# Optimization experiments

Hardware: AMD Instinct MI355X
Metric: run time of the kernel (lower is better)

## Reference

```python
import jax, jax.numpy as jnp
import numpy as np

T_CONST = 0.1

def _hardtanh(w):
    # F.hardtanh(w, min_val=1e-10, max_val=1)
    return jnp.clip(w, 1e-10, 1.0)

def _forward(inp, hn, w_str2str, w_str2snr, w_m12m1, w_m12str, w_thal2m1,
             w_m12thal, w_thal2str, w_str2stn, w_stn2snr, w_snr2thal,
             str2str_fixed, inp_weight, mean_w, mean_b, std_w, std_b, hid_dim):
    H = hid_dim
    H5 = 5 * H
    Z = jnp.zeros((H, H), dtype=inp.dtype)
    n_inhib = int(0.3 * H)

    # Diagonal 'D' matrices realized as column scalings (D is diagonal)
    m12m1_d = jnp.concatenate([jnp.ones((H - n_inhib,)), -jnp.ones((n_inhib,))])

    # Block masks
    str2str_mask = jnp.zeros((H, H))
    m12str_mask = jnp.concatenate([jnp.ones((H, H - n_inhib)), jnp.zeros((H, n_inhib))], axis=1)
    str2stn_mask = jnp.concatenate([jnp.zeros((H, H // 2)), jnp.ones((H, H // 2))], axis=1)
    str2snr_mask = jnp.concatenate([jnp.ones((H, H // 2)), jnp.zeros((H, H // 2))], axis=1)

    # Region masks over the full 5H state
    thal_mask = jnp.concatenate([jnp.zeros((3 * H,)), jnp.ones((H,)), jnp.zeros((H,))])
    m1_mask = jnp.zeros((H5,))  # cat(zeros(4H), zeros(H)) in the source

    # Effective recurrent blocks (str2str_D = stn2snr_D = snr2thal_D = str2snr_D = -I)
    str2str_rec = -(str2str_mask * _hardtanh(w_str2str) + str2str_fixed)
    m12m1_rec = _hardtanh(w_m12m1) * m12m1_d[None, :]
    m12str_rec = m12str_mask * _hardtanh(w_m12str)
    str2snr_rec = -(str2snr_mask * _hardtanh(w_str2snr))
    thal2m1_rec = _hardtanh(w_thal2m1)
    m12thal_rec = _hardtanh(w_m12thal)
    thal2str_rec = _hardtanh(w_thal2str)
    str2stn_rec = str2stn_mask * _hardtanh(w_str2stn)
    stn2snr_rec = -_hardtanh(w_str2stn)  # NOTE: source uses str2stn weight here (faithful to original)
    snr2thal_rec = -_hardtanh(w_snr2thal)

    W_rec = jnp.concatenate([
        jnp.concatenate([str2str_rec, Z, Z, thal2str_rec, m12str_rec], axis=1),
        jnp.concatenate([str2stn_rec, Z, Z, Z, Z], axis=1),
        jnp.concatenate([str2snr_rec, stn2snr_rec, Z, Z, Z], axis=1),
        jnp.concatenate([Z, Z, snr2thal_rec, Z, m12thal_rec], axis=1),
        jnp.concatenate([Z, Z, Z, thal2m1_rec, m12m1_rec], axis=1),
    ], axis=0)  # [5H, 5H]

    # Precompute masked input drive for all timesteps: [T, B, 5H]
    u = jnp.einsum('bti,ih->tbh', inp, _hardtanh(inp_weight)) * thal_mask

    W_rec_T = W_rec.T

    def step(h, u_t):
        # (W_rec @ h.T).T == h @ W_rec.T
        h_new = jax.nn.relu((1.0 - T_CONST) * h + T_CONST * (h @ W_rec_T + u_t))
        return h_new, h_new

    _, hs = jax.lax.scan(step, hn[0], u)  # hs: [T, B, 5H]
    rnn_out = jnp.transpose(hs, (1, 0, 2))  # [B, T, 5H]
    hn_last = rnn_out[:, -1, :][None]  # [1, B, 5H]

    masked = rnn_out * m1_mask
    mean_out = masked @ mean_w + mean_b
    std_out = jnp.clip(masked @ std_w + std_b, -5.0, 10.0)
    return mean_out, std_out, rnn_out, hn_last


def setup_inputs() -> dict:
    H, B, T, I, A = 256, 64, 512, 4, 1
    H5 = 5 * H
    key = jax.random.key(0)
    ks = jax.random.split(key, 20)
    u01 = lambda k, shape, s: jax.random.uniform(k, shape, dtype=jnp.float32) * s
    inputs = {
        'inp': jax.random.uniform(ks[0], (B, T, I), dtype=jnp.float32),
        'hn': jnp.zeros((1, B, H5), dtype=jnp.float32),
        'w_str2str': u01(ks[1], (H, H), 0.01),
        'w_str2snr': u01(ks[2], (H, H), 0.01),
        'w_m12m1': u01(ks[3], (H, H), 0.01),
        'w_m12str': u01(ks[4], (H, H), 0.01),
        'w_thal2m1': u01(ks[5], (H, H), 0.01),
        'w_m12thal': u01(ks[6], (H, H), 0.01),
        'w_thal2str': u01(ks[7], (H, H), 0.01),
        'w_str2stn': u01(ks[8], (H, H), 0.01),
        'w_stn2snr': u01(ks[9], (H, H), 0.01),
        'w_snr2thal': u01(ks[10], (H, H), 0.01),
        'inp_weight': u01(ks[12], (I, H5), 0.1),
        'mean_w': jax.random.normal(ks[13], (H5, A), dtype=jnp.float32) * 0.02,
        'mean_b': jnp.zeros((A,), dtype=jnp.float32),
        'std_w': jax.random.normal(ks[14], (H5, A), dtype=jnp.float32) * 0.02,
        'std_b': jnp.zeros((A,), dtype=jnp.float32),
        'hid_dim': H,
    }
    keep = jax.random.bernoulli(ks[11], 0.15, (H, H)).astype(jnp.float32)
    inputs['str2str_fixed'] = u01(ks[15], (H, H), 0.01) * keep
    return inputs


def reference(inp, hn, w_str2str, w_str2snr, w_m12m1, w_m12str, w_thal2m1,
              w_m12thal, w_thal2str, w_str2stn, w_stn2snr, w_snr2thal,
              str2str_fixed, inp_weight, mean_w, mean_b, std_w, std_b, hid_dim):
    return _forward(inp, hn, w_str2str, w_str2snr, w_m12m1, w_m12str, w_thal2m1,
                    w_m12thal, w_thal2str, w_str2stn, w_stn2snr, w_snr2thal,
                    str2str_fixed, inp_weight, mean_w, mean_b, std_w, std_b, hid_dim)
```

## Files before the change

### kernel.cpp

```cpp
#include <hip/hip_runtime.h>

typedef unsigned short u16;
typedef unsigned long long u64;
typedef __bf16 v8bf __attribute__((ext_vector_type(8)));
typedef float f32x4 __attribute__((ext_vector_type(4)));
typedef u16 u16x4 __attribute__((ext_vector_type(4)));

#define H5 1280
#define TT 512
#define NBLK 80
#define SPL 81920

#define OFF_W0 0
#define OFF_W1 3276800
#define OFF_W2 6553600
#define OFF_HS 9830400
#define OFF_WIN 10813440
#define OFF_CNT 10817536

#define MFMA(a, b, c) __builtin_amdgcn_mfma_f32_16x16x32_bf16(a, b, c, 0, 0, 0)

__device__ __forceinline__ float htanh_(float x) {
  return fminf(fmaxf(x, 1e-10f), 1.0f);
}
__device__ __forceinline__ u16 f2b(float f) {
  unsigned u = __float_as_uint(f);
  return (u16)((u + 0x7fffu + ((u >> 16) & 1u)) >> 16);
}
__device__ __forceinline__ float b2f(u16 b) {
  return __uint_as_float(((unsigned)b) << 16);
}

__device__ __forceinline__ v8bf ald16(const u16* p) {
  union { u64 q[2]; v8bf v; } u;
  u.q[0] = __hip_atomic_load((const u64*)p, __ATOMIC_RELAXED, __HIP_MEMORY_SCOPE_AGENT);
  u.q[1] = __hip_atomic_load((const u64*)(p + 4), __ATOMIC_RELAXED, __HIP_MEMORY_SCOPE_AGENT);
  return u.v;
}
__device__ __forceinline__ void sth(u16* p, u16x4 v) {
  union { u16x4 s; u64 q; } u;
  u.s = v;
  __hip_atomic_store((u64*)p, u.q, __ATOMIC_RELAXED, __HIP_MEMORY_SCOPE_AGENT);
}

__global__ void build_w(const float* __restrict__ w_str2snr, const float* __restrict__ w_m12m1,
                        const float* __restrict__ w_m12str, const float* __restrict__ w_thal2m1,
                        const float* __restrict__ w_m12thal, const float* __restrict__ w_thal2str,
                        const float* __restrict__ w_str2stn, const float* __restrict__ w_snr2thal,
                        const float* __restrict__ fixedw, u16* __restrict__ W0,
                        u16* __restrict__ W1, u16* __restrict__ W2) {
  int idx = blockIdx.x * 256 + threadIdx.x;
  if (idx >= H5 * H5) return;
  int j = idx / H5, k = idx - j * H5;
  int jr = j >> 8, kr = k >> 8, kk = k & 255;
  int o = (j & 255) * 256 + kk;
  float w = 0.0f;
  if (jr == 0) {
    if (kr == 0) w = -fixedw[o];
    else if (kr == 3) w = htanh_(w_thal2str[o]);
    else if (kr == 4) w = (kk < 180) ? htanh_(w_m12str[o]) : 0.0f;
  } else if (jr == 1) {
    if (kr == 0) w = (kk >= 128) ? htanh_(w_str2stn[o]) : 0.0f;
  } else if (jr == 2) {
    if (kr == 0) w = (kk < 128) ? -htanh_(w_str2snr[o]) : 0.0f;
    else if (kr == 1) w = -htanh_(w_str2stn[o]);
  } else if (jr == 3) {
    if (kr == 2) w = -htanh_(w_snr2thal[o]);
    else if (kr == 4) w = htanh_(w_m12thal[o]);
  } else {
    if (kr == 3) w = htanh_(w_thal2m1[o]);
    else if (kr == 4) w = (kk < 180) ? htanh_(w_m12m1[o]) : -htanh_(w_m12m1[o]);
  }
  u16 c0 = f2b(w);  float r1 = w - b2f(c0);
  u16 c1 = f2b(r1); float r2 = r1 - b2f(c1);
  u16 c2 = f2b(r2);
  W0[idx] = c0; W1[idx] = c1; W2[idx] = c2;
}

__global__ void build_misc(const float* __restrict__ hn, const float* __restrict__ inp_weight,
                           const float* __restrict__ mean_b, const float* __restrict__ std_b,
                           float* __restrict__ out, u16* __restrict__ hs, float* __restrict__ Win) {
  int gid = blockIdx.x * 256 + threadIdx.x;
  if (gid < 65536) {
    out[gid] = (gid < 32768) ? mean_b[0] : fminf(10.0f, fmaxf(-5.0f, std_b[0]));
  } else if (gid < 65536 + SPL) {
    int i = gid - 65536;
    float v = hn[i];
    u16 c0 = f2b(v);  float r1 = v - b2f(c0);
    u16 c1 = f2b(r1); float r2 = r1 - b2f(c1);
    u16 c2 = f2b(r2);
    hs[i] = c0; hs[SPL + i] = c1; hs[2 * SPL + i] = c2;
  } else if (gid < 65536 + SPL + 1024) {
    int i = gid - 65536 - SPL;
    Win[i] = htanh_(inp_weight[(i >> 8) * H5 + 768 + (i & 255)]);
  }
}

template <int R> struct RC;
template <> struct RC<0> { static constexpr int kb[3] = {0, 768, 1024}; static constexpr int nch[3] = {8, 8, 8}; };
template <> struct RC<1> { static constexpr int kb[3] = {128, 0, 0};    static constexpr int nch[3] = {4, 0, 0}; };
template <> struct RC<2> { static constexpr int kb[3] = {0, 256, 0};    static constexpr int nch[3] = {4, 8, 0}; };
template <> struct RC<3> { static constexpr int kb[3] = {512, 1024, 0}; static constexpr int nch[3] = {8, 8, 0}; };
template <> struct RC<4> { static constexpr int kb[3] = {768, 1024, 0}; static constexpr int nch[3] = {8, 8, 0}; };

template <int R>
__device__ __forceinline__ f32x4 do_mm(const u16* __restrict__ hs_r, int b, int lk,
                                       const u16* __restrict__ w0r, const u16* __restrict__ w1r,
                                       const u16* __restrict__ w2r) {
  f32x4 A00 = {0.f, 0.f, 0.f, 0.f}, A01 = {0.f, 0.f, 0.f, 0.f}, A02 = {0.f, 0.f, 0.f, 0.f};
  f32x4 A10 = {0.f, 0.f, 0.f, 0.f}, A11 = {0.f, 0.f, 0.f, 0.f}, A20 = {0.f, 0.f, 0.f, 0.f};
#pragma unroll
  for (int q = 0; q < 3; ++q) {
    if (RC<R>::nch[q] > 0) {
      const int kbq = RC<R>::kb[q];
      const u16* hb = hs_r + (long)b * H5 + kbq + lk;
#pragma unroll
      for (int c = 0; c < RC<R>::nch[q]; ++c) {
        v8bf h0 = ald16(hb + c * 32);
        v8bf h1 = ald16(hb + SPL + c * 32);
        v8bf h2 = ald16(hb + 2 * SPL + c * 32);
        v8bf a0 = *(const v8bf*)(w0r + kbq + c * 32);
        v8bf a1 = *(const v8bf*)(w1r + kbq + c * 32);
        v8bf a2 = *(const v8bf*)(w2r + kbq + c * 32);
        A00 = MFMA(a0, h0, A00);
        A01 = MFMA(a0, h1, A01);
        A02 = MFMA(a0, h2, A02);
        A10 = MFMA(a1, h0, A10);
        A11 = MFMA(a1, h1, A11);
        A20 = MFMA(a2, h0, A20);
      }
    }
  }
  f32x4 acc;
#pragma unroll
  for (int rr = 0; rr < 4; ++rr)
    acc[rr] = ((A00[rr] + A10[rr]) + (A01[rr] + A11[rr])) + (A02[rr] + A20[rr]);
  return acc;
}

template <int R>
__device__ void pers_loop(int j0, int b, int lr, int hi, int lk,
                          const float* __restrict__ inp_b, const float* __restrict__ hn,
                          const u16* __restrict__ W0, const u16* __restrict__ W1,
                          const u16* __restrict__ W2, u16* __restrict__ hs,
                          float* __restrict__ rnn_b, float* __restrict__ hn_last,
                          const float* __restrict__ Win, unsigned* __restrict__ counter) {
  const long jrow = (long)(j0 + lr) * H5 + lk;
  const u16* w0r = W0 + jrow;
  const u16* w1r = W1 + jrow;
  const u16* w2r = W2 + jrow;

  float winreg[4][4];
  if constexpr (R == 3) {
#pragma unroll
    for (int i = 0; i < 4; ++i)
#pragma unroll
      for (int rr = 0; rr < 4; ++rr)
        winreg[i][rr] = Win[i * 256 + (j0 - 768) + hi * 4 + rr];
  }

  f32x4 hprev;
  {
    const float* hp = hn + (long)b * H5 + j0 + hi * 4;
#pragma unroll
    for (int rr = 0; rr < 4; ++rr) hprev[rr] = hp[rr];
  }

  const u64 ca = (u64)counter;

  for (int t = 0; t < TT; ++t) {
    const u16* hs_r = hs + (t & 1) * (3 * SPL);
    u16* hs_w = hs + ((t & 1) ^ 1) * (3 * SPL);

    f32x4 acc = do_mm<R>(hs_r, b, lk, w0r, w1r, w2r);

    if constexpr (R == 3) {
      const float* ip = inp_b + t * 4;
      float i0 = ip[0], i1 = ip[1], i2 = ip[2], i3 = ip[3];
#pragma unroll
      for (int rr = 0; rr < 4; ++rr)
        acc[rr] += i0 * winreg[0][rr] + i1 * winreg[1][rr] + i2 * winreg[2][rr] + i3 * winreg[3][rr];
    }

    f32x4 hnew;
#pragma unroll
    for (int rr = 0; rr < 4; ++rr)
      hnew[rr] = fmaxf(0.0f, 0.9f * hprev[rr] + 0.1f * acc[rr]);
    hprev = hnew;

    *(f32x4*)(rnn_b + (long)t * H5 + j0 + hi * 4) = hnew;

    if (t < TT - 1) {
      u16x4 s0, s1, s2;
#pragma unroll
      for (int rr = 0; rr < 4; ++rr) {
        float v = hnew[rr];
        u16 c0 = f2b(v);  float r1 = v - b2f(c0);
        u16 c1 = f2b(r1); float r2 = r1 - b2f(c1);
        s0[rr] = c0; s1[rr] = c1; s2[rr] = f2b(r2);
      }
      u16* hw = hs_w + (long)b * H5 + j0 + hi * 4;
      sth(hw, s0);
      sth(hw + SPL, s1);
      sth(hw + 2 * SPL, s2);

      asm volatile("s_waitcnt vmcnt(0)" ::: "memory");
      __syncthreads();
      if (threadIdx.x == 0) {
        unsigned old;
        asm volatile("global_atomic_add %0, %1, %2, off sc0 sc1\n\t"
                     "s_waitcnt vmcnt(0)"
                     : "=v"(old) : "v"(ca), "v"(1u) : "memory");
        const unsigned target = (unsigned)(t + 1) * NBLK;
        for (;;) {
          unsigned cur;
          asm volatile("global_load_dword %0, %1, off sc0 sc1\n\t"
                       "s_waitcnt vmcnt(0)"
                       : "=v"(cur) : "v"(ca) : "memory");
          if (cur >= target) break;
          __builtin_amdgcn_s_sleep(1);
        }
      }
      __syncthreads();
    } else {
      float* hl = hn_last + (long)b * H5 + j0 + hi * 4;
#pragma unroll
      for (int rr = 0; rr < 4; ++rr) hl[rr] = hnew[rr];
    }
  }
}

__global__ void __launch_bounds__(256, 1)
rnn_pers(const float* __restrict__ inp, const float* __restrict__ hn,
         const u16* __restrict__ W0, const u16* __restrict__ W1, const u16* __restrict__ W2,
         u16* __restrict__ hs, float* __restrict__ rnn, float* __restrict__ hn_last,
         const float* __restrict__ Win, unsigned* __restrict__ counter) {
  const int lane = threadIdx.x & 63;
  const int lr = lane & 15, hi = lane >> 4, lk = hi * 8;
  const int jt = blockIdx.x;
  const int bt = threadIdx.x >> 6;
  const int j0 = jt << 4;
  const int b = (bt << 4) + lr;
  float* rnn_b = rnn + (long)b * TT * H5;
  const float* inp_b = inp + (long)b * TT * 4;
  switch (jt >> 4) {
    case 0: pers_loop<0>(j0, b, lr, hi, lk, inp_b, hn, W0, W1, W2, hs, rnn_b, hn_last, Win, counter); break;
    case 1: pers_loop<1>(j0, b, lr, hi, lk, inp_b, hn, W0, W1, W2, hs, rnn_b, hn_last, Win, counter); break;
    case 2: pers_loop<2>(j0, b, lr, hi, lk, inp_b, hn, W0, W1, W2, hs, rnn_b, hn_last, Win, counter); break;
    case 3: pers_loop<3>(j0, b, lr, hi, lk, inp_b, hn, W0, W1, W2, hs, rnn_b, hn_last, Win, counter); break;
    default: pers_loop<4>(j0, b, lr, hi, lk, inp_b, hn, W0, W1, W2, hs, rnn_b, hn_last, Win, counter); break;
  }
}

template <int R>
__device__ void step_one(int t, int j0, int b, int lr, int hi, int lk,
                         const float* __restrict__ inp_b, const float* __restrict__ hn,
                         const u16* __restrict__ W0, const u16* __restrict__ W1,
                         const u16* __restrict__ W2, u16* __restrict__ hs,
                         float* __restrict__ rnn, float* __restrict__ rnn_b,
                         float* __restrict__ hn_last, const float* __restrict__ Win) {
  const long jrow = (long)(j0 + lr) * H5 + lk;
  const u16* hs_r = hs + (t & 1) * (3 * SPL);
  u16* hs_w = hs + ((t & 1) ^ 1) * (3 * SPL);

  f32x4 acc = do_mm<R>(hs_r, b, lk, W0 + jrow, W1 + jrow, W2 + jrow);

  if constexpr (R == 3) {
    float winreg[4][4];
#pragma unroll
    for (int i = 0; i < 4; ++i)
#pragma unroll
      for (int rr = 0; rr < 4; ++rr)
        winreg[i][rr] = Win[i * 256 + (j0 - 768) + hi * 4 + rr];
    const float* ip = inp_b + t * 4;
    float i0 = ip[0], i1 = ip[1], i2 = ip[2], i3 = ip[3];
#pragma unroll
    for (int rr = 0; rr < 4; ++rr)
      acc[rr] += i0 * winreg[0][rr] + i1 * winreg[1][rr] + i2 * winreg[2][rr] + i3 * winreg[3][rr];
  }

  f32x4 hprev;
  {
    const float* hp = (t == 0) ? (hn + (long)b * H5 + j0 + hi * 4)
                               : (rnn + ((long)b * TT + (t - 1)) * H5 + j0 + hi * 4);
#pragma unroll
    for (int rr = 0; rr < 4; ++rr) hprev[rr] = hp[rr];
  }
  f32x4 hnew;
#pragma unroll
  for (int rr = 0; rr < 4; ++rr)
    hnew[rr] = fmaxf(0.0f, 0.9f * hprev[rr] + 0.1f * acc[rr]);

  *(f32x4*)(rnn_b + (long)t * H5 + j0 + hi * 4) = hnew;
  if (t < TT - 1) {
    u16x4 s0, s1, s2;
#pragma unroll
    for (int rr = 0; rr < 4; ++rr) {
      float v = hnew[rr];
      u16 c0 = f2b(v);  float r1 = v - b2f(c0);
      u16 c1 = f2b(r1); float r2 = r1 - b2f(c1);
      s0[rr] = c0; s1[rr] = c1; s2[rr] = f2b(r2);
    }
    u16* hw = hs_w + (long)b * H5 + j0 + hi * 4;
    sth(hw, s0);
    sth(hw + SPL, s1);
    sth(hw + 2 * SPL, s2);
  } else {
    float* hl = hn_last + (long)b * H5 + j0 + hi * 4;
#pragma unroll
    for (int rr = 0; rr < 4; ++rr) hl[rr] = hnew[rr];
  }
}

__global__ void __launch_bounds__(256, 1)
rnn_step(const float* __restrict__ inp, const float* __restrict__ hn,
         const u16* __restrict__ W0, const u16* __restrict__ W1, const u16* __restrict__ W2,
         u16* __restrict__ hs, float* __restrict__ rnn, float* __restrict__ hn_last,
         const float* __restrict__ Win, int t) {
  const int lane = threadIdx.x & 63;
  const int lr = lane & 15, hi = lane >> 4, lk = hi * 8;
  const int jt = blockIdx.x;
  const int bt = threadIdx.x >> 6;
  const int j0 = jt << 4;
  const int b = (bt << 4) + lr;
  float* rnn_b = rnn + (long)b * TT * H5;
  const float* inp_b = inp + (long)b * TT * 4;
  switch (jt >> 4) {
    case 0: step_one<0>(t, j0, b, lr, hi, lk, inp_b, hn, W0, W1, W2, hs, rnn, rnn_b, hn_last, Win); break;
    case 1: step_one<1>(t, j0, b, lr, hi, lk, inp_b, hn, W0, W1, W2, hs, rnn, rnn_b, hn_last, Win); break;
    case 2: step_one<2>(t, j0, b, lr, hi, lk, inp_b, hn, W0, W1, W2, hs, rnn, rnn_b, hn_last, Win); break;
    case 3: step_one<3>(t, j0, b, lr, hi, lk, inp_b, hn, W0, W1, W2, hs, rnn, rnn_b, hn_last, Win); break;
    default: step_one<4>(t, j0, b, lr, hi, lk, inp_b, hn, W0, W1, W2, hs, rnn, rnn_b, hn_last, Win); break;
  }
}

extern "C" void kernel_launch(void* const* d_in, const int* in_sizes, int n_in,
                              void* d_out, int out_size, void* d_ws, size_t ws_size,
                              hipStream_t stream) {
  const float* inp        = (const float*)d_in[0];
  const float* hn         = (const float*)d_in[1];
  const float* w_str2snr  = (const float*)d_in[3];
  const float* w_m12m1    = (const float*)d_in[4];
  const float* w_m12str   = (const float*)d_in[5];
  const float* w_thal2m1  = (const float*)d_in[6];
  const float* w_m12thal  = (const float*)d_in[7];
  const float* w_thal2str = (const float*)d_in[8];
  const float* w_str2stn  = (const float*)d_in[9];
  const float* w_snr2thal = (const float*)d_in[11];
  const float* inp_weight = (const float*)d_in[12];
  const float* mean_b     = (const float*)d_in[14];
  const float* std_b      = (const float*)d_in[16];
  const float* fixedw     = (const float*)d_in[18];

  char* ws = (char*)d_ws;
  u16* W0 = (u16*)(ws + OFF_W0);
  u16* W1 = (u16*)(ws + OFF_W1);
  u16* W2 = (u16*)(ws + OFF_W2);
  u16* hsb = (u16*)(ws + OFF_HS);
  float* Win = (float*)(ws + OFF_WIN);
  unsigned* cnt = (unsigned*)(ws + OFF_CNT);

  float* out = (float*)d_out;
  float* rnn = out + 65536;
  float* hnl = out + 65536 + 41943040;

  hipMemsetAsync(cnt, 0, 128, stream);
  build_w<<<6400, 256, 0, stream>>>(w_str2snr, w_m12m1, w_m12str, w_thal2m1, w_m12thal,
                                    w_thal2str, w_str2stn, w_snr2thal, fixedw, W0, W1, W2);
  build_misc<<<581, 256, 0, stream>>>(hn, inp_weight, mean_b, std_b, out, hsb, Win);

  void* args[] = {(void*)&inp, (void*)&hn, (void*)&W0, (void*)&W1, (void*)&W2, (void*)&hsb,
                  (void*)&rnn, (void*)&hnl, (void*)&Win, (void*)&cnt};
  hipError_t e = hipLaunchCooperativeKernel((const void*)rnn_pers, dim3(NBLK), dim3(256),
                                            args, 0, stream);
  if (e != hipSuccess) {
    for (int t = 0; t < TT; ++t)
      rnn_step<<<NBLK, 256, 0, stream>>>(inp, hn, W0, W1, W2, hsb, rnn, hnl, Win, t);
  }
}
```

Baseline: 10.20 ms.

## Split grid barrier into four independent batch-group barriers and batch state loads

Blocks are remapped so each block covers 4 row tiles for a single 16-sample batch group, which means the recurrent dependency only spans the 20 blocks of the same group. Each group gets its own counter at a separate stride, so a block waits for 20 peers instead of all 80. The hidden-state loads for a whole K segment are also issued together as dwordx4 loads with a single wait before the MFMAs, which helps hide latency. The costs are more registers and less reuse of weight rows across batch tiles within a block, since each block now reads four distinct weight row sets.

```diff
diff --git a/kernel.cpp b/kernel.cpp
--- a/kernel.cpp
+++ b/kernel.cpp
@@ -9,6 +9,7 @@
 #define H5 1280
 #define TT 512
 #define NBLK 80
+#define GBLK 20
 #define SPL 81920
 
 #define OFF_W0 0
@@ -31,11 +32,10 @@
   return __uint_as_float(((unsigned)b) << 16);
 }
 
-__device__ __forceinline__ v8bf ald16(const u16* p) {
-  union { u64 q[2]; v8bf v; } u;
-  u.q[0] = __hip_atomic_load((const u64*)p, __ATOMIC_RELAXED, __HIP_MEMORY_SCOPE_AGENT);
-  u.q[1] = __hip_atomic_load((const u64*)(p + 4), __ATOMIC_RELAXED, __HIP_MEMORY_SCOPE_AGENT);
-  return u.v;
+__device__ __forceinline__ v8bf ldh16(const u16* p) {
+  v8bf v;
+  asm volatile("global_load_dwordx4 %0, %1, off sc0 sc1" : "=v"(v) : "v"(p) : "memory");
+  return v;
 }
 __device__ __forceinline__ void sth(u16* p, u16x4 v) {
   union { u16x4 s; u64 q; } u;
@@ -114,20 +114,26 @@
     if (RC<R>::nch[q] > 0) {
       const int kbq = RC<R>::kb[q];
       const u16* hb = hs_r + (long)b * H5 + kbq + lk;
+      v8bf h0[8], h1[8], h2[8];
 #pragma unroll
       for (int c = 0; c < RC<R>::nch[q]; ++c) {
-        v8bf h0 = ald16(hb + c * 32);
-        v8bf h1 = ald16(hb + SPL + c * 32);
-        v8bf h2 = ald16(hb + 2 * SPL + c * 32);
+        h0[c] = ldh16(hb + c * 32);
+        h1[c] = ldh16(hb + SPL + c * 32);
+        h2[c] = ldh16(hb + 2 * SPL + c * 32);
+      }
+      asm volatile("s_waitcnt vmcnt(0)" ::: "memory");
+      __builtin_amdgcn_sched_barrier(0);
+#pragma unroll
+      for (int c = 0; c < RC<R>::nch[q]; ++c) {
         v8bf a0 = *(const v8bf*)(w0r + kbq + c * 32);
         v8bf a1 = *(const v8bf*)(w1r + kbq + c * 32);
         v8bf a2 = *(const v8bf*)(w2r + kbq + c * 32);
-        A00 = MFMA(a0, h0, A00);
-        A01 = MFMA(a0, h1, A01);
-        A02 = MFMA(a0, h2, A02);
-        A10 = MFMA(a1, h0, A10);
-        A11 = MFMA(a1, h1, A11);
-        A20 = MFMA(a2, h0, A20);
+        A00 = MFMA(a0, h0[c], A00);
+        A01 = MFMA(a0, h1[c], A01);
+        A02 = MFMA(a0, h2[c], A02);
+        A10 = MFMA(a1, h0[c], A10);
+        A11 = MFMA(a1, h1[c], A11);
+        A20 = MFMA(a2, h0[c], A20);
       }
     }
   }
@@ -144,7 +150,7 @@
                           const u16* __restrict__ W0, const u16* __restrict__ W1,
                           const u16* __restrict__ W2, u16* __restrict__ hs,
                           float* __restrict__ rnn_b, float* __restrict__ hn_last,
-                          const float* __restrict__ Win, unsigned* __restrict__ counter) {
+                          const float* __restrict__ Win, unsigned* __restrict__ ctr) {
   const long jrow = (long)(j0 + lr) * H5 + lk;
   const u16* w0r = W0 + jrow;
   const u16* w1r = W1 + jrow;
@@ -166,7 +172,7 @@
     for (int rr = 0; rr < 4; ++rr) hprev[rr] = hp[rr];
   }
 
-  const u64 ca = (u64)counter;
+  const u64 ca = (u64)ctr;
 
   for (int t = 0; t < TT; ++t) {
     const u16* hs_r = hs + (t & 1) * (3 * SPL);
@@ -211,14 +217,14 @@
         asm volatile("global_atomic_add %0, %1, %2, off sc0 sc1\n\t"
                      "s_waitcnt vmcnt(0)"
                      : "=v"(old) : "v"(ca), "v"(1u) : "memory");
-        const unsigned target = (unsigned)(t + 1) * NBLK;
+        const unsigned target = (unsigned)(t + 1) * GBLK;
         for (;;) {
           unsigned cur;
           asm volatile("global_load_dword %0, %1, off sc0 sc1\n\t"
                        "s_waitcnt vmcnt(0)"
                        : "=v"(cur) : "v"(ca) : "memory");
           if (cur >= target) break;
-          __builtin_amdgcn_s_sleep(1);
+          __builtin_amdgcn_s_sleep(2);
         }
       }
       __syncthreads();
@@ -234,21 +240,24 @@
 rnn_pers(const float* __restrict__ inp, const float* __restrict__ hn,
          const u16* __restrict__ W0, const u16* __restrict__ W1, const u16* __restrict__ W2,
          u16* __restrict__ hs, float* __restrict__ rnn, float* __restrict__ hn_last,
-         const float* __restrict__ Win, unsigned* __restrict__ counter) {
+         const float* __restrict__ Win, unsigned* __restrict__ cnt, int cstride) {
   const int lane = threadIdx.x & 63;
   const int lr = lane & 15, hi = lane >> 4, lk = hi * 8;
-  const int jt = blockIdx.x;
-  const int bt = threadIdx.x >> 6;
+  const int g = blockIdx.x & 3;
+  const int i = blockIdx.x >> 2;
+  const int w = threadIdx.x >> 6;
+  const int jt = i * 4 + w;
   const int j0 = jt << 4;
-  const int b = (bt << 4) + lr;
+  const int b = (g << 4) + lr;
+  unsigned* ctr = cnt + g * cstride;
   float* rnn_b = rnn + (long)b * TT * H5;
   const float* inp_b = inp + (long)b * TT * 4;
-  switch (jt >> 4) {
-    case 0: pers_loop<0>(j0, b, lr, hi, lk, inp_b, hn, W0, W1, W2, hs, rnn_b, hn_last, Win, counter); break;
-    case 1: pers_loop<1>(j0, b, lr, hi, lk, inp_b, hn, W0, W1, W2, hs, rnn_b, hn_last, Win, counter); break;
-    case 2: pers_loop<2>(j0, b, lr, hi, lk, inp_b, hn, W0, W1, W2, hs, rnn_b, hn_last, Win, counter); break;
-    case 3: pers_loop<3>(j0, b, lr, hi, lk, inp_b, hn, W0, W1, W2, hs, rnn_b, hn_last, Win, counter); break;
-    default: pers_loop<4>(j0, b, lr, hi, lk, inp_b, hn, W0, W1, W2, hs, rnn_b, hn_last, Win, counter); break;
+  switch (i >> 2) {
+    case 0: pers_loop<0>(j0, b, lr, hi, lk, inp_b, hn, W0, W1, W2, hs, rnn_b, hn_last, Win, ctr); break;
+    case 1: pers_loop<1>(j0, b, lr, hi, lk, inp_b, hn, W0, W1, W2, hs, rnn_b, hn_last, Win, ctr); break;
+    case 2: pers_loop<2>(j0, b, lr, hi, lk, inp_b, hn, W0, W1, W2, hs, rnn_b, hn_last, Win, ctr); break;
+    case 3: pers_loop<3>(j0, b, lr, hi, lk, inp_b, hn, W0, W1, W2, hs, rnn_b, hn_last, Win, ctr); break;
+    default: pers_loop<4>(j0, b, lr, hi, lk, inp_b, hn, W0, W1, W2, hs, rnn_b, hn_last, Win, ctr); break;
   }
 }
 
@@ -319,13 +328,15 @@
          const float* __restrict__ Win, int t) {
   const int lane = threadIdx.x & 63;
   const int lr = lane & 15, hi = lane >> 4, lk = hi * 8;
-  const int jt = blockIdx.x;
-  const int bt = threadIdx.x >> 6;
+  const int g = blockIdx.x & 3;
+  const int i = blockIdx.x >> 2;
+  const int w = threadIdx.x >> 6;
+  const int jt = i * 4 + w;
   const int j0 = jt << 4;
-  const int b = (bt << 4) + lr;
+  const int b = (g << 4) + lr;
   float* rnn_b = rnn + (long)b * TT * H5;
   const float* inp_b = inp + (long)b * TT * 4;
-  switch (jt >> 4) {
+  switch (i >> 2) {
     case 0: step_one<0>(t, j0, b, lr, hi, lk, inp_b, hn, W0, W1, W2, hs, rnn, rnn_b, hn_last, Win); break;
     case 1: step_one<1>(t, j0, b, lr, hi, lk, inp_b, hn, W0, W1, W2, hs, rnn, rnn_b, hn_last, Win); break;
     case 2: step_one<2>(t, j0, b, lr, hi, lk, inp_b, hn, W0, W1, W2, hs, rnn, rnn_b, hn_last, Win); break;
@@ -360,17 +371,22 @@
   float* Win = (float*)(ws + OFF_WIN);
   unsigned* cnt = (unsigned*)(ws + OFF_CNT);
 
+  int cstride;
+  size_t cbytes;
+  if (ws_size >= (size_t)OFF_CNT + 1024) { cstride = 64; cbytes = 1024; }
+  else                                   { cstride = 8;  cbytes = 128;  }
+
   float* out = (float*)d_out;
   float* rnn = out + 65536;
   float* hnl = out + 65536 + 41943040;
 
-  hipMemsetAsync(cnt, 0, 128, stream);
+  hipMemsetAsync(cnt, 0, cbytes, stream);
   build_w<<<6400, 256, 0, stream>>>(w_str2snr, w_m12m1, w_m12str, w_thal2m1, w_m12thal,
                                     w_thal2str, w_str2stn, w_snr2thal, fixedw, W0, W1, W2);
   build_misc<<<581, 256, 0, stream>>>(hn, inp_weight, mean_b, std_b, out, hsb, Win);
 
   void* args[] = {(void*)&inp, (void*)&hn, (void*)&W0, (void*)&W1, (void*)&W2, (void*)&hsb,
-                  (void*)&rnn, (void*)&hnl, (void*)&Win, (void*)&cnt};
+                  (void*)&rnn, (void*)&hnl, (void*)&Win, (void*)&cnt, (void*)&cstride};
   hipError_t e = hipLaunchCooperativeKernel((const void*)rnn_pers, dim3(NBLK), dim3(256),
                                             args, 0, stream);
   if (e != hipSuccess) {
```

Result: faster. 8.959 ms (-12.2%).

## Replace persistent cooperative kernel with per-timestep launches and regrouped block mapping

Applied to the files above, without the earlier changes.

Removes the persistent cooperative kernel and its atomic-counter grid barrier, and instead launches one rnn_step kernel per timestep, with kernel boundaries providing the synchronisation. State loads and stores become plain vector accesses instead of relaxed atomics. The block-to-work mapping changes so each block's four waves cover four consecutive row tiles for one batch group, giving blocks a shared batch slice and a contiguous row range. The cost is 512 kernel launches with their launch latency in place of the in-kernel spin barrier.

```diff
diff --git a/kernel.cpp b/kernel.cpp
--- a/kernel.cpp
+++ b/kernel.cpp
@@ -1,7 +1,6 @@
 #include <hip/hip_runtime.h>
 
 typedef unsigned short u16;
-typedef unsigned long long u64;
 typedef __bf16 v8bf __attribute__((ext_vector_type(8)));
 typedef float f32x4 __attribute__((ext_vector_type(4)));
 typedef u16 u16x4 __attribute__((ext_vector_type(4)));
@@ -16,7 +15,6 @@
 #define OFF_W2 6553600
 #define OFF_HS 9830400
 #define OFF_WIN 10813440
-#define OFF_CNT 10817536
 
 #define MFMA(a, b, c) __builtin_amdgcn_mfma_f32_16x16x32_bf16(a, b, c, 0, 0, 0)
 
@@ -29,18 +27,6 @@
 }
 __device__ __forceinline__ float b2f(u16 b) {
   return __uint_as_float(((unsigned)b) << 16);
-}
-
-__device__ __forceinline__ v8bf ald16(const u16* p) {
-  union { u64 q[2]; v8bf v; } u;
-  u.q[0] = __hip_atomic_load((const u64*)p, __ATOMIC_RELAXED, __HIP_MEMORY_SCOPE_AGENT);
-  u.q[1] = __hip_atomic_load((const u64*)(p + 4), __ATOMIC_RELAXED, __HIP_MEMORY_SCOPE_AGENT);
-  return u.v;
-}
-__device__ __forceinline__ void sth(u16* p, u16x4 v) {
-  union { u16x4 s; u64 q; } u;
-  u.s = v;
-  __hip_atomic_store((u64*)p, u.q, __ATOMIC_RELAXED, __HIP_MEMORY_SCOPE_AGENT);
 }
 
 __global__ void build_w(const float* __restrict__ w_str2snr, const float* __restrict__ w_m12m1,
@@ -116,9 +102,9 @@
       const u16* hb = hs_r + (long)b * H5 + kbq + lk;
 #pragma unroll
       for (int c = 0; c < RC<R>::nch[q]; ++c) {
-        v8bf h0 = ald16(hb + c * 32);
-        v8bf h1 = ald16(hb + SPL + c * 32);
-        v8bf h2 = ald16(hb + 2 * SPL + c * 32);
+        v8bf h0 = *(const v8bf*)(hb + c * 32);
+        v8bf h1 = *(const v8bf*)(hb + SPL + c * 32);
+        v8bf h2 = *(const v8bf*)(hb + 2 * SPL + c * 32);
         v8bf a0 = *(const v8bf*)(w0r + kbq + c * 32);
         v8bf a1 = *(const v8bf*)(w1r + kbq + c * 32);
         v8bf a2 = *(const v8bf*)(w2r + kbq + c * 32);
@@ -139,120 +125,6 @@
 }
 
 template <int R>
-__device__ void pers_loop(int j0, int b, int lr, int hi, int lk,
-                          const float* __restrict__ inp_b, const float* __restrict__ hn,
-                          const u16* __restrict__ W0, const u16* __restrict__ W1,
-                          const u16* __restrict__ W2, u16* __restrict__ hs,
-                          float* __restrict__ rnn_b, float* __restrict__ hn_last,
-                          const float* __restrict__ Win, unsigned* __restrict__ counter) {
-  const long jrow = (long)(j0 + lr) * H5 + lk;
-  const u16* w0r = W0 + jrow;
-  const u16* w1r = W1 + jrow;
-  const u16* w2r = W2 + jrow;
-
-  float winreg[4][4];
-  if constexpr (R == 3) {
-#pragma unroll
-    for (int i = 0; i < 4; ++i)
-#pragma unroll
-      for (int rr = 0; rr < 4; ++rr)
-        winreg[i][rr] = Win[i * 256 + (j0 - 768) + hi * 4 + rr];
-  }
-
-  f32x4 hprev;
-  {
-    const float* hp = hn + (long)b * H5 + j0 + hi * 4;
-#pragma unroll
-    for (int rr = 0; rr < 4; ++rr) hprev[rr] = hp[rr];
-  }
-
-  const u64 ca = (u64)counter;
-
-  for (int t = 0; t < TT; ++t) {
-    const u16* hs_r = hs + (t & 1) * (3 * SPL);
-    u16* hs_w = hs + ((t & 1) ^ 1) * (3 * SPL);
-
-    f32x4 acc = do_mm<R>(hs_r, b, lk, w0r, w1r, w2r);
-
-    if constexpr (R == 3) {
-      const float* ip = inp_b + t * 4;
-      float i0 = ip[0], i1 = ip[1], i2 = ip[2], i3 = ip[3];
-#pragma unroll
-      for (int rr = 0; rr < 4; ++rr)
-        acc[rr] += i0 * winreg[0][rr] + i1 * winreg[1][rr] + i2 * winreg[2][rr] + i3 * winreg[3][rr];
-    }
-
-    f32x4 hnew;
-#pragma unroll
-    for (int rr = 0; rr < 4; ++rr)
-      hnew[rr] = fmaxf(0.0f, 0.9f * hprev[rr] + 0.1f * acc[rr]);
-    hprev = hnew;
-
-    *(f32x4*)(rnn_b + (long)t * H5 + j0 + hi * 4) = hnew;
-
-    if (t < TT - 1) {
-      u16x4 s0, s1, s2;
-#pragma unroll
-      for (int rr = 0; rr < 4; ++rr) {
-        float v = hnew[rr];
-        u16 c0 = f2b(v);  float r1 = v - b2f(c0);
-        u16 c1 = f2b(r1); float r2 = r1 - b2f(c1);
-        s0[rr] = c0; s1[rr] = c1; s2[rr] = f2b(r2);
-      }
-      u16* hw = hs_w + (long)b * H5 + j0 + hi * 4;
-      sth(hw, s0);
-      sth(hw + SPL, s1);
-      sth(hw + 2 * SPL, s2);
-
-      asm volatile("s_waitcnt vmcnt(0)" ::: "memory");
-      __syncthreads();
-      if (threadIdx.x == 0) {
-        unsigned old;
-        asm volatile("global_atomic_add %0, %1, %2, off sc0 sc1\n\t"
-                     "s_waitcnt vmcnt(0)"
-                     : "=v"(old) : "v"(ca), "v"(1u) : "memory");
-        const unsigned target = (unsigned)(t + 1) * NBLK;
-        for (;;) {
-          unsigned cur;
-          asm volatile("global_load_dword %0, %1, off sc0 sc1\n\t"
-                       "s_waitcnt vmcnt(0)"
-                       : "=v"(cur) : "v"(ca) : "memory");
-          if (cur >= target) break;
-          __builtin_amdgcn_s_sleep(1);
-        }
-      }
-      __syncthreads();
-    } else {
-      float* hl = hn_last + (long)b * H5 + j0 + hi * 4;
-#pragma unroll
-      for (int rr = 0; rr < 4; ++rr) hl[rr] = hnew[rr];
-    }
-  }
-}
-
-__global__ void __launch_bounds__(256, 1)
-rnn_pers(const float* __restrict__ inp, const float* __restrict__ hn,
-         const u16* __restrict__ W0, const u16* __restrict__ W1, const u16* __restrict__ W2,
-         u16* __restrict__ hs, float* __restrict__ rnn, float* __restrict__ hn_last,
-         const float* __restrict__ Win, unsigned* __restrict__ counter) {
-  const int lane = threadIdx.x & 63;
-  const int lr = lane & 15, hi = lane >> 4, lk = hi * 8;
-  const int jt = blockIdx.x;
-  const int bt = threadIdx.x >> 6;
-  const int j0 = jt << 4;
-  const int b = (bt << 4) + lr;
-  float* rnn_b = rnn + (long)b * TT * H5;
-  const float* inp_b = inp + (long)b * TT * 4;
-  switch (jt >> 4) {
-    case 0: pers_loop<0>(j0, b, lr, hi, lk, inp_b, hn, W0, W1, W2, hs, rnn_b, hn_last, Win, counter); break;
-    case 1: pers_loop<1>(j0, b, lr, hi, lk, inp_b, hn, W0, W1, W2, hs, rnn_b, hn_last, Win, counter); break;
-    case 2: pers_loop<2>(j0, b, lr, hi, lk, inp_b, hn, W0, W1, W2, hs, rnn_b, hn_last, Win, counter); break;
-    case 3: pers_loop<3>(j0, b, lr, hi, lk, inp_b, hn, W0, W1, W2, hs, rnn_b, hn_last, Win, counter); break;
-    default: pers_loop<4>(j0, b, lr, hi, lk, inp_b, hn, W0, W1, W2, hs, rnn_b, hn_last, Win, counter); break;
-  }
-}
-
-template <int R>
 __device__ void step_one(int t, int j0, int b, int lr, int hi, int lk,
                          const float* __restrict__ inp_b, const float* __restrict__ hn,
                          const u16* __restrict__ W0, const u16* __restrict__ W1,
@@ -302,9 +174,9 @@
       s0[rr] = c0; s1[rr] = c1; s2[rr] = f2b(r2);
     }
     u16* hw = hs_w + (long)b * H5 + j0 + hi * 4;
-    sth(hw, s0);
-    sth(hw + SPL, s1);
-    sth(hw + 2 * SPL, s2);
+    *(u16x4*)(hw) = s0;
+    *(u16x4*)(hw + SPL) = s1;
+    *(u16x4*)(hw + 2 * SPL) = s2;
   } else {
     float* hl = hn_last + (long)b * H5 + j0 + hi * 4;
 #pragma unroll
@@ -319,13 +191,15 @@
          const float* __restrict__ Win, int t) {
   const int lane = threadIdx.x & 63;
   const int lr = lane & 15, hi = lane >> 4, lk = hi * 8;
-  const int jt = blockIdx.x;
-  const int bt = threadIdx.x >> 6;
+  const int g = blockIdx.x & 3;
+  const int i = blockIdx.x >> 2;
+  const int w = threadIdx.x >> 6;
+  const int jt = i * 4 + w;
   const int j0 = jt << 4;
-  const int b = (bt << 4) + lr;
+  const int b = (g << 4) + lr;
   float* rnn_b = rnn + (long)b * TT * H5;
   const float* inp_b = inp + (long)b * TT * 4;
-  switch (jt >> 4) {
+  switch (i >> 2) {
     case 0: step_one<0>(t, j0, b, lr, hi, lk, inp_b, hn, W0, W1, W2, hs, rnn, rnn_b, hn_last, Win); break;
     case 1: step_one<1>(t, j0, b, lr, hi, lk, inp_b, hn, W0, W1, W2, hs, rnn, rnn_b, hn_last, Win); break;
     case 2: step_one<2>(t, j0, b, lr, hi, lk, inp_b, hn, W0, W1, W2, hs, rnn, rnn_b, hn_last, Win); break;
@@ -358,23 +232,15 @@
   u16* W2 = (u16*)(ws + OFF_W2);
   u16* hsb = (u16*)(ws + OFF_HS);
   float* Win = (float*)(ws + OFF_WIN);
-  unsigned* cnt = (unsigned*)(ws + OFF_CNT);
 
   float* out = (float*)d_out;
   float* rnn = out + 65536;
   float* hnl = out + 65536 + 41943040;
 
-  hipMemsetAsync(cnt, 0, 128, stream);
   build_w<<<6400, 256, 0, stream>>>(w_str2snr, w_m12m1, w_m12str, w_thal2m1, w_m12thal,
                                     w_thal2str, w_str2stn, w_snr2thal, fixedw, W0, W1, W2);
   build_misc<<<581, 256, 0, stream>>>(hn, inp_weight, mean_b, std_b, out, hsb, Win);
 
-  void* args[] = {(void*)&inp, (void*)&hn, (void*)&W0, (void*)&W1, (void*)&W2, (void*)&hsb,
-                  (void*)&rnn, (void*)&hnl, (void*)&Win, (void*)&cnt};
-  hipError_t e = hipLaunchCooperativeKernel((const void*)rnn_pers, dim3(NBLK), dim3(256),
-                                            args, 0, stream);
-  if (e != hipSuccess) {
-    for (int t = 0; t < TT; ++t)
-      rnn_step<<<NBLK, 256, 0, stream>>>(inp, hn, W0, W1, W2, hsb, rnn, hnl, Win, t);
-  }
-}
+  for (int t = 0; t < TT; ++t)
+    rnn_step<<<NBLK, 256, 0, stream>>>(inp, hn, W0, W1, W2, hsb, rnn, hnl, Win, t);
+}
```

New measurement: 9.301 ms. 8.8% less time.
